# Performance work log

Measured on AMD Instinct MI355X. Metric: run time of the kernel, lower is better.

## Reference

```python
import jax, jax.numpy as jnp
import numpy as np

D_MODEL = 768
N_HEADS = 8
HEAD_DIM = D_MODEL // N_HEADS
D_FF = 3072
EPS = 1e-5


def _layernorm(x, g, b):
    mu = jnp.mean(x, axis=-1, keepdims=True)
    var = jnp.var(x, axis=-1, keepdims=True)
    return (x - mu) * jax.lax.rsqrt(var + EPS) * g + b


def setup_inputs() -> dict:
    key = jax.random.key(0)
    ks = jax.random.split(key, 12)
    s = 0.02
    return {
        "x": jax.random.normal(ks[0], (2, 4096, D_MODEL), dtype=jnp.float32),
        "w_qkv": jax.random.normal(ks[1], (D_MODEL, 3 * D_MODEL), dtype=jnp.float32) * s,
        "b_qkv": jnp.zeros((3 * D_MODEL,), dtype=jnp.float32),
        "w_out": jax.random.normal(ks[2], (D_MODEL, D_MODEL), dtype=jnp.float32) * s,
        "b_out": jnp.zeros((D_MODEL,), dtype=jnp.float32),
        "w_ff1": jax.random.normal(ks[3], (D_MODEL, D_FF), dtype=jnp.float32) * s,
        "b_ff1": jnp.zeros((D_FF,), dtype=jnp.float32),
        "w_ff2": jax.random.normal(ks[4], (D_FF, D_MODEL), dtype=jnp.float32) * s,
        "b_ff2": jnp.zeros((D_MODEL,), dtype=jnp.float32),
        "g1": jnp.ones((D_MODEL,), dtype=jnp.float32),
        "be1": jnp.zeros((D_MODEL,), dtype=jnp.float32),
        "g2": jnp.ones((D_MODEL,), dtype=jnp.float32),
        "be2": jnp.zeros((D_MODEL,), dtype=jnp.float32),
    }


def reference(x, w_qkv, b_qkv, w_out, b_out, w_ff1, b_ff1, w_ff2, b_ff2, g1, be1, g2, be2):
    B, S, D = x.shape
    qkv = x @ w_qkv + b_qkv  # [B,S,3D]
    q, k, v = jnp.split(qkv, 3, axis=-1)
    # [B,H,S,d]
    q = q.reshape(B, S, N_HEADS, HEAD_DIM).transpose(0, 2, 1, 3)
    k = k.reshape(B, S, N_HEADS, HEAD_DIM).transpose(0, 2, 1, 3)
    v = v.reshape(B, S, N_HEADS, HEAD_DIM).transpose(0, 2, 1, 3)
    scores = jnp.einsum("bhqd,bhkd->bhqk", q, k) / np.sqrt(HEAD_DIM).astype(np.float32)
    attn = jax.nn.softmax(scores, axis=-1)
    out = jnp.einsum("bhqk,bhkd->bhqd", attn, v)
    out = out.transpose(0, 2, 1, 3).reshape(B, S, D)
    out = out @ w_out + b_out
    x = _layernorm(x + out, g1, be1)
    h = jax.nn.gelu(x @ w_ff1 + b_ff1, approximate=False)
    ffn = h @ w_ff2 + b_ff2
    return _layernorm(x + ffn, g2, be2)
```

## Files before the change

### kernel.cpp

```cpp
#include <hip/hip_runtime.h>
#include <hip/hip_bf16.h>
#include <stdint.h>


typedef __attribute__((ext_vector_type(8))) short bf16x8;
typedef __attribute__((ext_vector_type(4))) short bf16x4;
typedef __attribute__((ext_vector_type(4))) float f32x4;

#define MFMA_BF16(a, b, c) __builtin_amdgcn_mfma_f32_16x16x32_bf16((a), (b), (c), 0, 0, 0)

__device__ __forceinline__ short f2bs(float f) {
  return __builtin_bit_cast(short, __float2bfloat16(f));
}
__device__ __forceinline__ float bs2f(short s) {
  union { unsigned u; float f; } v;
  v.u = ((unsigned)(unsigned short)s) << 16;
  return v.f;
}

__device__ __forceinline__ void gload16(const void* g, void* l) {
  __builtin_amdgcn_global_load_lds(
      (const __attribute__((address_space(1))) unsigned int*)g,
      (__attribute__((address_space(3))) unsigned int*)l, 16, 0, 0);
}

__device__ __forceinline__ unsigned ldsoff(const void* p) {
  return (unsigned)(uintptr_t)p;
}

#define TRD(dst, base, off) \
  asm volatile("ds_read_b64_tr_b16 %0, %1 offset:" #off : "=v"(dst) : "v"(base) : "memory")

__global__ __launch_bounds__(256) void transpose_cast(const float* __restrict__ W,
                                                      short* __restrict__ Wt,
                                                      int K, int N) {
  __shared__ float tile[32][33];
  const int n0 = blockIdx.x * 32, k0 = blockIdx.y * 32;
  const int tx = threadIdx.x & 31, ty = threadIdx.x >> 5;
#pragma unroll
  for (int i = 0; i < 4; ++i)
    tile[ty + i * 8][tx] = W[(size_t)(k0 + ty + i * 8) * N + n0 + tx];
  __syncthreads();
#pragma unroll
  for (int i = 0; i < 4; ++i)
    Wt[(size_t)(n0 + ty + i * 8) * K + k0 + tx] = f2bs(tile[tx][ty + i * 8]);
}

__global__ __launch_bounds__(256) void cast_bf16(const float* __restrict__ x,
                                                 short* __restrict__ y, int n4) {
  const int i = blockIdx.x * 256 + threadIdx.x;
  if (i < n4) {
    const float4 v = *(const float4*)(x + (size_t)i * 4);
    short4 o;
    o.x = f2bs(v.x); o.y = f2bs(v.y); o.z = f2bs(v.z); o.w = f2bs(v.w);
    *(short4*)(y + (size_t)i * 4) = o;
  }
}

template <int EPI>
__global__ __launch_bounds__(256) void gemm_bt(const short* __restrict__ A,
                                               const short* __restrict__ Bt,
                                               const float* __restrict__ bias,
                                               void* __restrict__ outp,
                                               int N, int K) {
  __shared__ __align__(16) short la[128 * 32];
  __shared__ __align__(16) short lb[128 * 32];
  const int tid = threadIdx.x;
  const int lane = tid & 63, w = tid >> 6;
  const int lo = lane & 15, hi = lane >> 4;
  const int wr = w >> 1, wc = w & 1;

  const unsigned gdx = gridDim.x;
  const unsigned nwg = gdx * gridDim.y;
  unsigned lin = blockIdx.y * gdx + blockIdx.x;
  if ((nwg & 7u) == 0u) lin = (lin & 7u) * (nwg >> 3) + (lin >> 3);
  const unsigned by = lin / gdx, bx = lin - by * gdx;
  const int m0 = by * 128, n0 = bx * 128;

  f32x4 acc[4][4] = {};

  const int srow = tid >> 2;
  const int scol = (tid & 3) * 8;
  char* la_dst = (char*)la + w * 1024;
  char* lb_dst = (char*)lb + w * 1024;

  for (int kt = 0; kt < K; kt += 32) {
    __syncthreads();
#pragma unroll
    for (int c = 0; c < 2; ++c) {
      gload16(A  + (size_t)(m0 + c * 64 + srow) * K + kt + scol, la_dst + c * 4096);
      gload16(Bt + (size_t)(n0 + c * 64 + srow) * K + kt + scol, lb_dst + c * 4096);
    }
    __syncthreads();
    bf16x8 af[4], bfr[4];
#pragma unroll
    for (int i = 0; i < 4; ++i) {
      af[i]  = *(const bf16x8*)(la + (wr * 64 + i * 16 + lo) * 32 + hi * 8);
      bfr[i] = *(const bf16x8*)(lb + (wc * 64 + i * 16 + lo) * 32 + hi * 8);
    }
#pragma unroll
    for (int mi = 0; mi < 4; ++mi)
#pragma unroll
      for (int ni = 0; ni < 4; ++ni)
        acc[mi][ni] = MFMA_BF16(af[mi], bfr[ni], acc[mi][ni]);
  }

  const int rb = m0 + wr * 64, cb = n0 + wc * 64;
#pragma unroll
  for (int ni = 0; ni < 4; ++ni) {
    const int col = cb + ni * 16 + lo;
    const float bc = bias[col];
#pragma unroll
    for (int mi = 0; mi < 4; ++mi) {
#pragma unroll
      for (int r = 0; r < 4; ++r) {
        const int row = rb + mi * 16 + hi * 4 + r;
        const float v = acc[mi][ni][r] + bc;
        if constexpr (EPI == 0) {
          const int which = col / 768, rem = col - which * 768;
          const int hh = rem / 96, d = rem - hh * 96;
          const int bb = row >> 12, ss = row & 4095;
          ((short*)outp)[((size_t)((which * 2 + bb) * 8 + hh) * 4096 + ss) * 96 + d] = f2bs(v);
        } else if constexpr (EPI == 1) {
          ((float*)outp)[(size_t)row * N + col] = v;
        } else {
          const float ge = 0.5f * v * (1.f + erff(v * 0.70710678118654752f));
          ((short*)outp)[(size_t)row * N + col] = f2bs(ge);
        }
      }
    }
  }
}

__global__ __launch_bounds__(256, 2) void attn_fwd(const short* __restrict__ qkv,
                                                   short* __restrict__ out) {
  constexpr int SEQ = 4096;
  constexpr int NT = SEQ / 64;
  constexpr float SCALE = 0.10206207261596575f;
  const int qt = blockIdx.x, h = blockIdx.y, b = blockIdx.z;
  const int tid = threadIdx.x;
  const int lane = tid & 63, w = tid >> 6;
  const int lo = lane & 15, hi = lane >> 4;

  const size_t headsz = (size_t)SEQ * 96;
  const short* Qh = qkv + (size_t)((0 * 2 + b) * 8 + h) * headsz;
  const short* Kh = qkv + (size_t)((1 * 2 + b) * 8 + h) * headsz;
  const short* Vh = qkv + (size_t)((2 * 2 + b) * 8 + h) * headsz;

  __shared__ __align__(16) short k_lds[2][6144];
  __shared__ __align__(16) short v_lds[2][6144];
  __shared__ __align__(16) short p_lds[4][2048];

  int voff[3];
#pragma unroll
  for (int t = 0; t < 3; ++t) {
    const int c = t * 256 + tid;
    const int kq = c / 48, rem = c - kq * 48;
    const int dhi = rem >> 3, rem2 = rem & 7;
    voff[t] = (kq * 4 + (rem2 >> 1)) * 96 + dhi * 16 + (rem2 & 1) * 8;
  }

  const int qbase = qt * 128 + w * 32;
  bf16x8 qf[2][3];
#pragma unroll
  for (int f = 0; f < 2; ++f)
#pragma unroll
    for (int dk = 0; dk < 3; ++dk) {
      bf16x8 v = *(const bf16x8*)(Qh + (size_t)(qbase + f * 16 + lo) * 96 + dk * 32 + hi * 8);
#pragma unroll
      for (int i = 0; i < 8; ++i) v[i] = f2bs(bs2f(v[i]) * SCALE);
      qf[f][dk] = v;
    }

  f32x4 o[2][6] = {};
  float mrow[2][4] = {};
  float lpart[2][4] = {};
  bool escaped = false;

  auto stage = [&](int t_next, int buf) {
    const short* Kt = Kh + (size_t)t_next * 6144;
    const short* Vt = Vh + (size_t)t_next * 6144;
    char* kd = (char*)k_lds[buf] + w * 1024;
    char* vd = (char*)v_lds[buf] + w * 1024;
#pragma unroll
    for (int t = 0; t < 3; ++t) {
      gload16((const char*)Kt + (t * 256 + tid) * 16, kd + t * 4096);
      gload16((const char*)Vt + (size_t)voff[t] * 2, vd + t * 4096);
    }
  };

  stage(0, 0);

  for (int kt = 0; kt < NT; ++kt) {
    const int cur = kt & 1;
    __syncthreads();
    if (kt + 1 < NT) stage(kt + 1, cur ^ 1);

    f32x4 s[2][4] = {};
    const short* kb = k_lds[cur];
#pragma unroll
    for (int dk = 0; dk < 3; ++dk)
#pragma unroll
      for (int c = 0; c < 4; ++c) {
        const bf16x8 kf = *(const bf16x8*)(kb + (c * 16 + lo) * 96 + dk * 32 + hi * 8);
#pragma unroll
        for (int f = 0; f < 2; ++f)
          s[f][c] = MFMA_BF16(qf[f][dk], kf, s[f][c]);
      }

    float tm = s[0][0][0];
#pragma unroll
    for (int f = 0; f < 2; ++f)
#pragma unroll
      for (int c = 0; c < 4; ++c)
#pragma unroll
        for (int r = 0; r < 4; ++r) tm = fmaxf(tm, s[f][c][r]);

    if (!__all(tm <= 8.0f)) {
      escaped = true;
#pragma unroll
      for (int f = 0; f < 2; ++f)
#pragma unroll
        for (int r = 0; r < 4; ++r) {
          float rm = fmaxf(fmaxf(s[f][0][r], s[f][1][r]), fmaxf(s[f][2][r], s[f][3][r]));
          rm = fmaxf(rm, __shfl_xor(rm, 1));
          rm = fmaxf(rm, __shfl_xor(rm, 2));
          rm = fmaxf(rm, __shfl_xor(rm, 4));
          rm = fmaxf(rm, __shfl_xor(rm, 8));
          const float mn = fmaxf(mrow[f][r], rm);
          const float al = __expf(mrow[f][r] - mn);
          mrow[f][r] = mn;
          lpart[f][r] *= al;
#pragma unroll
          for (int n = 0; n < 6; ++n) o[f][n][r] *= al;
        }
    }
    if (escaped) {
#pragma unroll
      for (int f = 0; f < 2; ++f)
#pragma unroll
        for (int c = 0; c < 4; ++c)
#pragma unroll
        for (int r = 0; r < 4; ++r) s[f][c][r] = __expf(s[f][c][r] - mrow[f][r]);
    } else {
#pragma unroll
      for (int f = 0; f < 2; ++f)
#pragma unroll
        for (int c = 0; c < 4; ++c)
#pragma unroll
        for (int r = 0; r < 4; ++r) s[f][c][r] = __expf(s[f][c][r]);
    }

    short* pw = p_lds[w];
#pragma unroll
    for (int f = 0; f < 2; ++f)
#pragma unroll
      for (int c = 0; c < 4; ++c) {
#pragma unroll
        for (int r = 0; r < 4; ++r) lpart[f][r] += s[f][c][r];
        short4 pk;
        pk.x = f2bs(s[f][c][0]);
        pk.y = f2bs(s[f][c][1]);
        pk.z = f2bs(s[f][c][2]);
        pk.w = f2bs(s[f][c][3]);
        *(short4*)(pw + (c * 4 + (lo >> 2)) * 128 + f * 64 + (lo & 3) * 16 + hi * 4) = pk;
      }

    const unsigned vb = ldsoff(v_lds[cur]) + (unsigned)(hi * 1536 + lo * 2);
    const unsigned pb = ldsoff(p_lds[w]) + (unsigned)(hi * 512 + lo * 2);

    {
      bf16x4 va[6], vbh[6], pa0[2], pa1[2];
      TRD(va[0], vb, 0);     TRD(vbh[0], vb, 768);
      TRD(va[1], vb, 128);   TRD(vbh[1], vb, 896);
      TRD(va[2], vb, 256);   TRD(vbh[2], vb, 1024);
      TRD(va[3], vb, 384);   TRD(vbh[3], vb, 1152);
      TRD(va[4], vb, 512);   TRD(vbh[4], vb, 1280);
      TRD(va[5], vb, 640);   TRD(vbh[5], vb, 1408);
      TRD(pa0[0], pb, 0);    TRD(pa1[0], pb, 256);
      TRD(pa0[1], pb, 128);  TRD(pa1[1], pb, 384);
      asm volatile("s_waitcnt lgkmcnt(0)" ::: "memory");
      __builtin_amdgcn_sched_barrier(0);
      __builtin_amdgcn_s_setprio(1);
#pragma unroll
      for (int f = 0; f < 2; ++f) {
        const bf16x8 pf = __builtin_shufflevector(pa0[f], pa1[f], 0, 1, 2, 3, 4, 5, 6, 7);
#pragma unroll
        for (int n = 0; n < 6; ++n) {
          const bf16x8 vf = __builtin_shufflevector(va[n], vbh[n], 0, 1, 2, 3, 4, 5, 6, 7);
          o[f][n] = MFMA_BF16(pf, vf, o[f][n]);
        }
      }
      __builtin_amdgcn_s_setprio(0);
    }
    {
      bf16x4 va[6], vbh[6], pa0[2], pa1[2];
      TRD(va[0], vb, 6144);  TRD(vbh[0], vb, 6912);
      TRD(va[1], vb, 6272);  TRD(vbh[1], vb, 7040);
      TRD(va[2], vb, 6400);  TRD(vbh[2], vb, 7168);
      TRD(va[3], vb, 6528);  TRD(vbh[3], vb, 7296);
      TRD(va[4], vb, 6656);  TRD(vbh[4], vb, 7424);
      TRD(va[5], vb, 6784);  TRD(vbh[5], vb, 7552);
      TRD(pa0[0], pb, 2048); TRD(pa1[0], pb, 2304);
      TRD(pa0[1], pb, 2176); TRD(pa1[1], pb, 2432);
      asm volatile("s_waitcnt lgkmcnt(0)" ::: "memory");
      __builtin_amdgcn_sched_barrier(0);
      __builtin_amdgcn_s_setprio(1);
#pragma unroll
      for (int f = 0; f < 2; ++f) {
        const bf16x8 pf = __builtin_shufflevector(pa0[f], pa1[f], 0, 1, 2, 3, 4, 5, 6, 7);
#pragma unroll
        for (int n = 0; n < 6; ++n) {
          const bf16x8 vf = __builtin_shufflevector(va[n], vbh[n], 0, 1, 2, 3, 4, 5, 6, 7);
          o[f][n] = MFMA_BF16(pf, vf, o[f][n]);
        }
      }
      __builtin_amdgcn_s_setprio(0);
    }
  }

  float inv[2][4];
#pragma unroll
  for (int f = 0; f < 2; ++f)
#pragma unroll
    for (int r = 0; r < 4; ++r) {
      float l = lpart[f][r];
      l += __shfl_xor(l, 1);
      l += __shfl_xor(l, 2);
      l += __shfl_xor(l, 4);
      l += __shfl_xor(l, 8);
      inv[f][r] = 1.f / l;
    }
#pragma unroll
  for (int f = 0; f < 2; ++f)
#pragma unroll
    for (int n = 0; n < 6; ++n)
#pragma unroll
      for (int r = 0; r < 4; ++r) {
        const int q = qbase + f * 16 + hi * 4 + r;
        out[((size_t)(b * SEQ + q)) * 768 + h * 96 + n * 16 + lo] = f2bs(o[f][n][r] * inv[f][r]);
      }
}

template <bool WB>
__global__ __launch_bounds__(192) void ln_residual(const float* __restrict__ xa,
                                                   const float* __restrict__ xr,
                                                   const float* __restrict__ g,
                                                   const float* __restrict__ be,
                                                   float* __restrict__ outf,
                                                   short* __restrict__ outb) {
  const int row = blockIdx.x, t = threadIdx.x;
  const size_t base = (size_t)row * 768 + t * 4;
  const float4 a = *(const float4*)(xa + base);
  const float4 bl = *(const float4*)(xr + base);
  const float v0 = a.x + bl.x, v1 = a.y + bl.y, v2 = a.z + bl.z, v3 = a.w + bl.w;
  float s = v0 + v1 + v2 + v3;
  float q = v0 * v0 + v1 * v1 + v2 * v2 + v3 * v3;
#pragma unroll
  for (int m = 32; m; m >>= 1) {
    s += __shfl_xor(s, m);
    q += __shfl_xor(q, m);
  }
  __shared__ float red[2][3];
  const int w = t >> 6;
  if ((t & 63) == 0) { red[0][w] = s; red[1][w] = q; }
  __syncthreads();
  s = red[0][0] + red[0][1] + red[0][2];
  q = red[1][0] + red[1][1] + red[1][2];
  const float mu = s * (1.f / 768.f);
  const float var = q * (1.f / 768.f) - mu * mu;
  const float rstd = rsqrtf(var + 1e-5f);
  const int c = t * 4;
  const float4 gg = *(const float4*)(g + c);
  const float4 bb = *(const float4*)(be + c);
  float y0 = (v0 - mu) * rstd * gg.x + bb.x;
  float y1 = (v1 - mu) * rstd * gg.y + bb.y;
  float y2 = (v2 - mu) * rstd * gg.z + bb.z;
  float y3 = (v3 - mu) * rstd * gg.w + bb.w;
  float4 ov = {y0, y1, y2, y3};
  *(float4*)(outf + base) = ov;
  if constexpr (WB) {
    short4 ob;
    ob.x = f2bs(y0); ob.y = f2bs(y1); ob.z = f2bs(y2); ob.w = f2bs(y3);
    *(short4*)(outb + base) = ob;
  }
}

extern "C" void kernel_launch(void* const* d_in, const int* in_sizes, int n_in,
                              void* d_out, int out_size, void* d_ws, size_t ws_size,
                              hipStream_t stream) {
  const float* x     = (const float*)d_in[0];
  const float* w_qkv = (const float*)d_in[1];
  const float* b_qkv = (const float*)d_in[2];
  const float* w_out = (const float*)d_in[3];
  const float* b_out = (const float*)d_in[4];
  const float* w_ff1 = (const float*)d_in[5];
  const float* b_ff1 = (const float*)d_in[6];
  const float* w_ff2 = (const float*)d_in[7];
  const float* b_ff2 = (const float*)d_in[8];
  const float* g1  = (const float*)d_in[9];
  const float* be1 = (const float*)d_in[10];
  const float* g2  = (const float*)d_in[11];
  const float* be2 = (const float*)d_in[12];

  char* ws = (char*)d_ws;
  size_t off = 0;
  auto take = [&](size_t bytes) {
    char* p = ws + off;
    off += (bytes + 255) & ~(size_t)255;
    return p;
  };
  short* wqkv_t = (short*)take((size_t)2304 * 768 * 2);
  short* wout_t = (short*)take((size_t)768 * 768 * 2);
  short* wff1_t = (short*)take((size_t)3072 * 768 * 2);
  short* wff2_t = (short*)take((size_t)768 * 3072 * 2);
  short* xb     = (short*)take((size_t)8192 * 768 * 2);
  short* qkv    = (short*)take((size_t)3 * 2 * 8 * 4096 * 96 * 2);
  short* ao     = (short*)take((size_t)8192 * 768 * 2);
  short* x1b    = (short*)take((size_t)8192 * 768 * 2);
  float* x1     = (float*)take((size_t)8192 * 768 * 4);
  if (ws_size < off) return;

  float* proj = (float*)qkv;
  short* hbuf = xb;
  float* ff2o = (float*)ao;

  cast_bf16<<<dim3(6144), dim3(256), 0, stream>>>(x, xb, 8192 * 768 / 4);
  transpose_cast<<<dim3(2304 / 32, 768 / 32), dim3(256), 0, stream>>>(w_qkv, wqkv_t, 768, 2304);
  transpose_cast<<<dim3(768 / 32, 768 / 32), dim3(256), 0, stream>>>(w_out, wout_t, 768, 768);
  transpose_cast<<<dim3(3072 / 32, 768 / 32), dim3(256), 0, stream>>>(w_ff1, wff1_t, 768, 3072);
  transpose_cast<<<dim3(768 / 32, 3072 / 32), dim3(256), 0, stream>>>(w_ff2, wff2_t, 3072, 768);

  gemm_bt<0><<<dim3(2304 / 128, 8192 / 128), dim3(256), 0, stream>>>(xb, wqkv_t, b_qkv, qkv, 2304, 768);

  attn_fwd<<<dim3(32, 8, 2), dim3(256), 0, stream>>>(qkv, ao);

  gemm_bt<1><<<dim3(768 / 128, 8192 / 128), dim3(256), 0, stream>>>(ao, wout_t, b_out, proj, 768, 768);

  ln_residual<true><<<dim3(8192), dim3(192), 0, stream>>>(x, proj, g1, be1, x1, x1b);

  gemm_bt<2><<<dim3(3072 / 128, 8192 / 128), dim3(256), 0, stream>>>(x1b, wff1_t, b_ff1, hbuf, 3072, 768);

  gemm_bt<1><<<dim3(768 / 128, 8192 / 128), dim3(256), 0, stream>>>(hbuf, wff2_t, b_ff2, ff2o, 768, 3072);

  ln_residual<false><<<dim3(8192), dim3(192), 0, stream>>>(x1, ff2o, g2, be2, (float*)d_out, nullptr);
}
```

Measured before the change: 384.7 us.

## Double-buffer GEMM LDS tiles and switch attention softmax to exp2

The GEMM now stages the next K tile into a second LDS buffer while the current tile feeds the MFMAs, with one barrier per iteration instead of two. This hides global-load latency behind compute, at the cost of doubling GEMM LDS use. The attention kernel folds log2(e) into the Q pre-scale and uses exp2f, with a matching threshold for the max-skip path. This removes a multiply from each exponential.

Result: slower. 404.3 us (+5.1%).

```diff
diff --git a/kernel.cpp b/kernel.cpp
--- a/kernel.cpp
+++ b/kernel.cpp
@@ -63,8 +63,8 @@
                                                const float* __restrict__ bias,
                                                void* __restrict__ outp,
                                                int N, int K) {
-  __shared__ __align__(16) short la[128 * 32];
-  __shared__ __align__(16) short lb[128 * 32];
+  __shared__ __align__(16) short la[2][128 * 32];
+  __shared__ __align__(16) short lb[2][128 * 32];
   const int tid = threadIdx.x;
   const int lane = tid & 63, w = tid >> 6;
   const int lo = lane & 15, hi = lane >> 4;
@@ -81,22 +81,28 @@
 
   const int srow = tid >> 2;
   const int scol = (tid & 3) * 8;
-  char* la_dst = (char*)la + w * 1024;
-  char* lb_dst = (char*)lb + w * 1024;
-
-  for (int kt = 0; kt < K; kt += 32) {
+
+  auto stage = [&](int kt, int buf) {
+#pragma unroll
+    for (int c = 0; c < 2; ++c) {
+      gload16(A  + (size_t)(m0 + c * 64 + srow) * K + kt + scol,
+              (char*)la[buf] + w * 1024 + c * 4096);
+      gload16(Bt + (size_t)(n0 + c * 64 + srow) * K + kt + scol,
+              (char*)lb[buf] + w * 1024 + c * 4096);
+    }
+  };
+
+  stage(0, 0);
+  const int nk = K >> 5;
+  for (int t = 0; t < nk; ++t) {
+    const int cur = t & 1;
     __syncthreads();
-#pragma unroll
-    for (int c = 0; c < 2; ++c) {
-      gload16(A  + (size_t)(m0 + c * 64 + srow) * K + kt + scol, la_dst + c * 4096);
-      gload16(Bt + (size_t)(n0 + c * 64 + srow) * K + kt + scol, lb_dst + c * 4096);
-    }
-    __syncthreads();
+    if (t + 1 < nk) stage((t + 1) << 5, cur ^ 1);
     bf16x8 af[4], bfr[4];
 #pragma unroll
     for (int i = 0; i < 4; ++i) {
-      af[i]  = *(const bf16x8*)(la + (wr * 64 + i * 16 + lo) * 32 + hi * 8);
-      bfr[i] = *(const bf16x8*)(lb + (wc * 64 + i * 16 + lo) * 32 + hi * 8);
+      af[i]  = *(const bf16x8*)(la[cur] + (wr * 64 + i * 16 + lo) * 32 + hi * 8);
+      bfr[i] = *(const bf16x8*)(lb[cur] + (wc * 64 + i * 16 + lo) * 32 + hi * 8);
     }
 #pragma unroll
     for (int mi = 0; mi < 4; ++mi)
@@ -136,7 +142,8 @@
                                                    short* __restrict__ out) {
   constexpr int SEQ = 4096;
   constexpr int NT = SEQ / 64;
-  constexpr float SCALE = 0.10206207261596575f;
+  constexpr float SCALE2 = 0.10206207261596575f * 1.44269504088896f;
+  constexpr float THR2 = 11.5415603f;
   const int qt = blockIdx.x, h = blockIdx.y, b = blockIdx.z;
   const int tid = threadIdx.x;
   const int lane = tid & 63, w = tid >> 6;
@@ -168,7 +175,7 @@
     for (int dk = 0; dk < 3; ++dk) {
       bf16x8 v = *(const bf16x8*)(Qh + (size_t)(qbase + f * 16 + lo) * 96 + dk * 32 + hi * 8);
 #pragma unroll
-      for (int i = 0; i < 8; ++i) v[i] = f2bs(bs2f(v[i]) * SCALE);
+      for (int i = 0; i < 8; ++i) v[i] = f2bs(bs2f(v[i]) * SCALE2);
       qf[f][dk] = v;
     }
 
@@ -216,7 +223,7 @@
 #pragma unroll
         for (int r = 0; r < 4; ++r) tm = fmaxf(tm, s[f][c][r]);
 
-    if (!__all(tm <= 8.0f)) {
+    if (!__all(tm <= THR2)) {
       escaped = true;
 #pragma unroll
       for (int f = 0; f < 2; ++f)
@@ -228,7 +235,7 @@
           rm = fmaxf(rm, __shfl_xor(rm, 4));
           rm = fmaxf(rm, __shfl_xor(rm, 8));
           const float mn = fmaxf(mrow[f][r], rm);
-          const float al = __expf(mrow[f][r] - mn);
+          const float al = exp2f(mrow[f][r] - mn);
           mrow[f][r] = mn;
           lpart[f][r] *= al;
 #pragma unroll
@@ -241,14 +248,14 @@
 #pragma unroll
         for (int c = 0; c < 4; ++c)
 #pragma unroll
-        for (int r = 0; r < 4; ++r) s[f][c][r] = __expf(s[f][c][r] - mrow[f][r]);
+        for (int r = 0; r < 4; ++r) s[f][c][r] = exp2f(s[f][c][r] - mrow[f][r]);
     } else {
 #pragma unroll
       for (int f = 0; f < 2; ++f)
 #pragma unroll
         for (int c = 0; c < 4; ++c)
 #pragma unroll
-        for (int r = 0; r < 4; ++r) s[f][c][r] = __expf(s[f][c][r]);
+        for (int r = 0; r < 4; ++r) s[f][c][r] = exp2f(s[f][c][r]);
     }
 
     short* pw = p_lds[w];
```
